# Performance work log

Hardware: AMD Instinct MI355X
Metric: run time of the kernel (lower is better)

The kernel has to match this reference:

```python
import jax, jax.numpy as jnp
import numpy as np

BETA = 0.25


def setup_inputs() -> dict:
    key = jax.random.key(0)
    k1, k2 = jax.random.split(key)
    x = jax.random.normal(k1, (32, 64, 64, 64), dtype=jnp.float32)
    # tf.random_uniform_initializer default: uniform in [-0.05, 0.05]
    embeddings = jax.random.uniform(k2, (64, 512), dtype=jnp.float32, minval=-0.05, maxval=0.05)
    return {"x": x, "embeddings": embeddings}


def reference(x, embeddings):
    D = embeddings.shape[0]
    flat = x.reshape(-1, D)  # [N, D]
    # squared euclidean distances via the matmul expansion: [N, K]
    distances = (
        jnp.sum(flat * flat, axis=1, keepdims=True)
        - 2.0 * (flat @ embeddings)
        + jnp.sum(embeddings * embeddings, axis=0, keepdims=True)
    )
    codes = jnp.argmin(distances, axis=1)  # [N]
    # direct gather of codebook rows (math-equivalent to one_hot @ embeddings.T)
    quantized = embeddings.T[codes].reshape(x.shape)
    loss = (
        jnp.mean((jax.lax.stop_gradient(x) - quantized) ** 2)
        + BETA * jnp.mean((x - jax.lax.stop_gradient(quantized)) ** 2)
    )
    # straight-through estimator
    out = x + jax.lax.stop_gradient(quantized - x)
    return out, loss
```

## Files before the change

kernel.cpp:

```cpp
#include <hip/hip_runtime.h>
#include <cstddef>

#define D 64
#define K 512
#define NROWS (32*64*64)
#define RPB 128
#define NBLK (NROWS / RPB)
#define NOUT 8388608


__global__ __launch_bounds__(256) void vq_prep(const float* __restrict__ emb,
                                               float* __restrict__ eT,
                                               float* __restrict__ enorm) {
    const int k = blockIdx.x * blockDim.x + threadIdx.x;
    if (k >= K) return;
    float nrm = 0.f;
#pragma unroll
    for (int d = 0; d < D; ++d) {
        const float v = emb[d * K + k];
        nrm = __fadd_rn(nrm, __fmul_rn(v, v));
        eT[k * D + d] = v;
    }
    enorm[k] = nrm;
}

__global__ __launch_bounds__(256, 4) void vq_main(const float* __restrict__ x,
                                                  const float* __restrict__ eT,
                                                  const float* __restrict__ enorm,
                                                  float* __restrict__ out,
                                                  float* __restrict__ partials) {
    __shared__ float s_dist[256];
    __shared__ int   s_idx[256];
    __shared__ float s_red[4];

    const int t    = threadIdx.x;
    const int wave = t >> 6;
    const int lane = t & 63;
    const int kh   = wave & 1;
    const int rl   = ((wave >> 1) << 6) + lane;
    const size_t row = (size_t)blockIdx.x * RPB + rl;

    float xr[64];
    const float4* __restrict__ xv = (const float4*)(x + row * D);
#pragma unroll
    for (int j = 0; j < 16; ++j) {
        const float4 v = xv[j];
        xr[4*j+0] = v.x; xr[4*j+1] = v.y; xr[4*j+2] = v.z; xr[4*j+3] = v.w;
    }

    float r0 = __fmul_rn(xr[0], xr[0]), r1 = __fmul_rn(xr[1], xr[1]);
    float r2 = __fmul_rn(xr[2], xr[2]), r3 = __fmul_rn(xr[3], xr[3]);
    float r4 = __fmul_rn(xr[4], xr[4]), r5 = __fmul_rn(xr[5], xr[5]);
    float r6 = __fmul_rn(xr[6], xr[6]), r7 = __fmul_rn(xr[7], xr[7]);
#pragma unroll
    for (int b = 1; b < 8; ++b) {
        r0 = __fadd_rn(r0, __fmul_rn(xr[8*b+0], xr[8*b+0]));
        r1 = __fadd_rn(r1, __fmul_rn(xr[8*b+1], xr[8*b+1]));
        r2 = __fadd_rn(r2, __fmul_rn(xr[8*b+2], xr[8*b+2]));
        r3 = __fadd_rn(r3, __fmul_rn(xr[8*b+3], xr[8*b+3]));
        r4 = __fadd_rn(r4, __fmul_rn(xr[8*b+4], xr[8*b+4]));
        r5 = __fadd_rn(r5, __fmul_rn(xr[8*b+5], xr[8*b+5]));
        r6 = __fadd_rn(r6, __fmul_rn(xr[8*b+6], xr[8*b+6]));
        r7 = __fadd_rn(r7, __fmul_rn(xr[8*b+7], xr[8*b+7]));
    }
    const float xnorm = __fadd_rn(__fadd_rn(__fadd_rn(r0, r1), __fadd_rn(r2, r3)),
                                  __fadd_rn(__fadd_rn(r4, r5), __fadd_rn(r6, r7)));

    const int kbase = __builtin_amdgcn_readfirstlane(kh << 8);
    float best = 3.4028235e38f;
    int   bidx = 0;
    for (int kk = 0; kk < 256; kk += 4) {
        const float4* __restrict__ e0 = (const float4*)(eT + (size_t)(kbase + kk + 0) * D);
        const float4* __restrict__ e1 = (const float4*)(eT + (size_t)(kbase + kk + 1) * D);
        const float4* __restrict__ e2 = (const float4*)(eT + (size_t)(kbase + kk + 2) * D);
        const float4* __restrict__ e3 = (const float4*)(eT + (size_t)(kbase + kk + 3) * D);
        float a00 = 0.f, a01 = 0.f, a02 = 0.f, a03 = 0.f;
        float a10 = 0.f, a11 = 0.f, a12 = 0.f, a13 = 0.f;
        float a20 = 0.f, a21 = 0.f, a22 = 0.f, a23 = 0.f;
        float a30 = 0.f, a31 = 0.f, a32 = 0.f, a33 = 0.f;
#pragma unroll
        for (int j = 0; j < 16; ++j) {
            const float4 v0 = e0[j], v1 = e1[j], v2 = e2[j], v3 = e3[j];
            const float x0 = xr[4*j+0], x1 = xr[4*j+1], x2 = xr[4*j+2], x3 = xr[4*j+3];
            a00 = fmaf(x0, v0.x, a00); a10 = fmaf(x0, v1.x, a10); a20 = fmaf(x0, v2.x, a20); a30 = fmaf(x0, v3.x, a30);
            a01 = fmaf(x1, v0.y, a01); a11 = fmaf(x1, v1.y, a11); a21 = fmaf(x1, v2.y, a21); a31 = fmaf(x1, v3.y, a31);
            a02 = fmaf(x2, v0.z, a02); a12 = fmaf(x2, v1.z, a12); a22 = fmaf(x2, v2.z, a22); a32 = fmaf(x2, v3.z, a32);
            a03 = fmaf(x3, v0.w, a03); a13 = fmaf(x3, v1.w, a13); a23 = fmaf(x3, v2.w, a23); a33 = fmaf(x3, v3.w, a33);
        }
        const float dot0 = __fadd_rn(__fadd_rn(a00, a01), __fadd_rn(a02, a03));
        const float dot1 = __fadd_rn(__fadd_rn(a10, a11), __fadd_rn(a12, a13));
        const float dot2 = __fadd_rn(__fadd_rn(a20, a21), __fadd_rn(a22, a23));
        const float dot3 = __fadd_rn(__fadd_rn(a30, a31), __fadd_rn(a32, a33));
        const float d0 = __fadd_rn(__fsub_rn(xnorm, __fmul_rn(2.f, dot0)), enorm[kbase + kk + 0]);
        const float d1 = __fadd_rn(__fsub_rn(xnorm, __fmul_rn(2.f, dot1)), enorm[kbase + kk + 1]);
        const float d2 = __fadd_rn(__fsub_rn(xnorm, __fmul_rn(2.f, dot2)), enorm[kbase + kk + 2]);
        const float d3 = __fadd_rn(__fsub_rn(xnorm, __fmul_rn(2.f, dot3)), enorm[kbase + kk + 3]);
        if (d0 < best) { best = d0; bidx = kbase + kk + 0; }
        if (d1 < best) { best = d1; bidx = kbase + kk + 1; }
        if (d2 < best) { best = d2; bidx = kbase + kk + 2; }
        if (d3 < best) { best = d3; bidx = kbase + kk + 3; }
    }

    s_dist[t] = best;
    s_idx[t]  = bidx;
    __syncthreads();
    const float ob = s_dist[t ^ 64];
    const int   oi = s_idx[t ^ 64];
    int fk = bidx;
    if (ob < best || (ob == best && oi < bidx)) fk = oi;

    const float4* __restrict__ eq = (const float4*)(eT + (size_t)fk * D + (kh << 5));
    float4* __restrict__ op = (float4*)(out + row * D + (kh << 5));
    float lacc = 0.f;
    const int xoff = kh << 5;
#pragma unroll
    for (int j = 0; j < 8; ++j) {
        const float4 q = eq[j];
        const float b0 = xr[xoff+4*j+0], b1 = xr[xoff+4*j+1], b2 = xr[xoff+4*j+2], b3 = xr[xoff+4*j+3];
        const float f0 = b0 - q.x, f1 = b1 - q.y, f2 = b2 - q.z, f3 = b3 - q.w;
        lacc = fmaf(f0, f0, lacc); lacc = fmaf(f1, f1, lacc);
        lacc = fmaf(f2, f2, lacc); lacc = fmaf(f3, f3, lacc);
        float4 o;
        o.x = __fadd_rn(b0, __fsub_rn(q.x, b0));
        o.y = __fadd_rn(b1, __fsub_rn(q.y, b1));
        o.z = __fadd_rn(b2, __fsub_rn(q.z, b2));
        o.w = __fadd_rn(b3, __fsub_rn(q.w, b3));
        op[j] = o;
    }

#pragma unroll
    for (int off = 32; off > 0; off >>= 1) lacc += __shfl_down(lacc, off);
    if (lane == 0) s_red[wave] = lacc;
    __syncthreads();
    if (t == 0) partials[blockIdx.x] = (s_red[0] + s_red[1]) + (s_red[2] + s_red[3]);
}

__global__ __launch_bounds__(256) void vq_finish(const float* __restrict__ partials,
                                                 float* __restrict__ loss_out) {
    __shared__ float s_red[4];
    const int t = threadIdx.x;
    float a = (partials[t] + partials[t + 256]) + (partials[t + 512] + partials[t + 768]);
#pragma unroll
    for (int off = 32; off > 0; off >>= 1) a += __shfl_down(a, off);
    if ((t & 63) == 0) s_red[t >> 6] = a;
    __syncthreads();
    if (t == 0) {
        const float S = (s_red[0] + s_red[1]) + (s_red[2] + s_red[3]);
        const float m = S / (float)NOUT;
        loss_out[0] = m + 0.25f * m;
    }
}

extern "C" void kernel_launch(void* const* d_in, const int* in_sizes, int n_in,
                              void* d_out, int out_size, void* d_ws, size_t ws_size,
                              hipStream_t stream) {
    const float* x   = (const float*)d_in[0];
    const float* emb = (const float*)d_in[1];
    float* out = (float*)d_out;
    float* ws  = (float*)d_ws;

    float* eT       = ws;
    float* enorm    = ws + 32768;
    float* partials = ws + 32768 + 512;

    vq_prep<<<2, 256, 0, stream>>>(emb, eT, enorm);
    vq_main<<<NBLK, 256, 0, stream>>>(x, eT, enorm, out, partials);
    vq_finish<<<1, 256, 0, stream>>>(partials, out + NOUT);
}
```

Before: 232.4 us.

## Split codebook four ways per row and coalesce the quantized output write

Each block now handles 64 rows, and the four waves each search a quarter of the codebook for the same rows, so the K dimension is split 4 ways instead of 2. The per-row winners are merged through shared memory. The epilogue is rewritten so 16 threads cooperate on each row, re-reading x and gathering the chosen code row with coalesced float4 accesses, which replaces the strided per-thread row writes. The changes aim to raise parallelism and improve store coalescing. In exchange, every wave redundantly loads the same x rows, x is read a second time in the epilogue, and the finish kernel now sums 2048 partials.

Result: faster. 221.1 us (-4.9%).

```diff
diff --git a/kernel.cpp b/kernel.cpp
--- a/kernel.cpp
+++ b/kernel.cpp
@@ -4,7 +4,7 @@
 #define D 64
 #define K 512
 #define NROWS (32*64*64)
-#define RPB 128
+#define RPB 64
 #define NBLK (NROWS / RPB)
 #define NOUT 8388608
 
@@ -31,14 +31,14 @@
                                                   float* __restrict__ partials) {
     __shared__ float s_dist[256];
     __shared__ int   s_idx[256];
+    __shared__ int   s_code[RPB];
     __shared__ float s_red[4];
 
     const int t    = threadIdx.x;
     const int wave = t >> 6;
     const int lane = t & 63;
-    const int kh   = wave & 1;
-    const int rl   = ((wave >> 1) << 6) + lane;
-    const size_t row = (size_t)blockIdx.x * RPB + rl;
+    const size_t rowbase = (size_t)blockIdx.x * RPB;
+    const size_t row = rowbase + lane;
 
     float xr[64];
     const float4* __restrict__ xv = (const float4*)(x + row * D);
@@ -46,6 +46,11 @@
     for (int j = 0; j < 16; ++j) {
         const float4 v = xv[j];
         xr[4*j+0] = v.x; xr[4*j+1] = v.y; xr[4*j+2] = v.z; xr[4*j+3] = v.w;
+    }
+#pragma unroll
+    for (int j = 0; j < 16; ++j) {
+        asm volatile("" : "+v"(xr[4*j+0]), "+v"(xr[4*j+1]),
+                          "+v"(xr[4*j+2]), "+v"(xr[4*j+3]));
     }
 
     float r0 = __fmul_rn(xr[0], xr[0]), r1 = __fmul_rn(xr[1], xr[1]);
@@ -66,10 +71,10 @@
     const float xnorm = __fadd_rn(__fadd_rn(__fadd_rn(r0, r1), __fadd_rn(r2, r3)),
                                   __fadd_rn(__fadd_rn(r4, r5), __fadd_rn(r6, r7)));
 
-    const int kbase = __builtin_amdgcn_readfirstlane(kh << 8);
+    const int kbase = __builtin_amdgcn_readfirstlane(wave << 7);
     float best = 3.4028235e38f;
     int   bidx = 0;
-    for (int kk = 0; kk < 256; kk += 4) {
+    for (int kk = 0; kk < 128; kk += 4) {
         const float4* __restrict__ e0 = (const float4*)(eT + (size_t)(kbase + kk + 0) * D);
         const float4* __restrict__ e1 = (const float4*)(eT + (size_t)(kbase + kk + 1) * D);
         const float4* __restrict__ e2 = (const float4*)(eT + (size_t)(kbase + kk + 2) * D);
@@ -104,28 +109,38 @@
     s_dist[t] = best;
     s_idx[t]  = bidx;
     __syncthreads();
-    const float ob = s_dist[t ^ 64];
-    const int   oi = s_idx[t ^ 64];
-    int fk = bidx;
-    if (ob < best || (ob == best && oi < bidx)) fk = oi;
+    if (t < RPB) {
+        float bb = s_dist[t];
+        int   bi = s_idx[t];
+#pragma unroll
+        for (int w = 1; w < 4; ++w) {
+            const float ob = s_dist[w * 64 + t];
+            const int   oi = s_idx[w * 64 + t];
+            if (ob < bb) { bb = ob; bi = oi; }
+        }
+        s_code[t] = bi;
+    }
+    __syncthreads();
 
-    const float4* __restrict__ eq = (const float4*)(eT + (size_t)fk * D + (kh << 5));
-    float4* __restrict__ op = (float4*)(out + row * D + (kh << 5));
+    const int c  = t & 15;
+    const int r0i = t >> 4;
     float lacc = 0.f;
-    const int xoff = kh << 5;
 #pragma unroll
-    for (int j = 0; j < 8; ++j) {
-        const float4 q = eq[j];
-        const float b0 = xr[xoff+4*j+0], b1 = xr[xoff+4*j+1], b2 = xr[xoff+4*j+2], b3 = xr[xoff+4*j+3];
-        const float f0 = b0 - q.x, f1 = b1 - q.y, f2 = b2 - q.z, f3 = b3 - q.w;
+    for (int i = 0; i < 4; ++i) {
+        const int r = r0i + 16 * i;
+        const int code = s_code[r];
+        const float4 q = *(const float4*)(eT + (size_t)code * D + 4 * c);
+        const float4 b = *(const float4*)(x + (rowbase + r) * D + 4 * c);
+        const float f0 = __fsub_rn(b.x, q.x), f1 = __fsub_rn(b.y, q.y);
+        const float f2 = __fsub_rn(b.z, q.z), f3 = __fsub_rn(b.w, q.w);
         lacc = fmaf(f0, f0, lacc); lacc = fmaf(f1, f1, lacc);
         lacc = fmaf(f2, f2, lacc); lacc = fmaf(f3, f3, lacc);
         float4 o;
-        o.x = __fadd_rn(b0, __fsub_rn(q.x, b0));
-        o.y = __fadd_rn(b1, __fsub_rn(q.y, b1));
-        o.z = __fadd_rn(b2, __fsub_rn(q.z, b2));
-        o.w = __fadd_rn(b3, __fsub_rn(q.w, b3));
-        op[j] = o;
+        o.x = __fadd_rn(b.x, __fsub_rn(q.x, b.x));
+        o.y = __fadd_rn(b.y, __fsub_rn(q.y, b.y));
+        o.z = __fadd_rn(b.z, __fsub_rn(q.z, b.z));
+        o.w = __fadd_rn(b.w, __fsub_rn(q.w, b.w));
+        *(float4*)(out + (rowbase + r) * D + 4 * c) = o;
     }
 
 #pragma unroll
@@ -139,7 +154,9 @@
                                                  float* __restrict__ loss_out) {
     __shared__ float s_red[4];
     const int t = threadIdx.x;
-    float a = (partials[t] + partials[t + 256]) + (partials[t + 512] + partials[t + 768]);
+    float a = 0.f;
+#pragma unroll
+    for (int i = 0; i < 8; ++i) a += partials[t + 256 * i];
 #pragma unroll
     for (int off = 32; off > 0; off >>= 1) a += __shfl_down(a, off);
     if ((t & 63) == 0) s_red[t >> 6] = a;
```
